# Performance work log

Measured on AMD Instinct MI355X. Metric: run time of the kernel, lower is better.

## Reference

```python
import jax, jax.numpy as jnp
import numpy as np

L, B, S, D, H, DK, F = 6, 4, 2048, 512, 8, 64, 2048


def setup_inputs() -> dict:
    key = jax.random.key(0)
    ks = iter(jax.random.split(key, 40))
    def rn(shape, scale=0.02):
        return jax.random.normal(next(ks), shape, jnp.float32) * scale
    inp = {
        "x": jax.random.normal(next(ks), (B, S, D), jnp.float32),
        "enc": jax.random.normal(next(ks), (B, S, D), jnp.float32),
    }
    for pre in ("sa", "ca"):
        inp[f"{pre}_wq"] = rn((L, D, H * DK)); inp[f"{pre}_bq"] = jnp.zeros((L, H * DK), jnp.float32)
        inp[f"{pre}_wk"] = rn((L, D, H * DK)); inp[f"{pre}_bk"] = jnp.zeros((L, H * DK), jnp.float32)
        inp[f"{pre}_wv"] = rn((L, D, H * DK)); inp[f"{pre}_bv"] = jnp.zeros((L, H * DK), jnp.float32)
        inp[f"{pre}_wo"] = rn((L, H * DK, D)); inp[f"{pre}_bo"] = jnp.zeros((L, D), jnp.float32)
    for i in (1, 2, 3):
        inp[f"ln{i}_g"] = jnp.ones((L, D), jnp.float32)
        inp[f"ln{i}_b"] = jnp.zeros((L, D), jnp.float32)
    inp["ff_w1"] = rn((L, D, F)); inp["ff_b1"] = jnp.zeros((L, F), jnp.float32)
    inp["ff_w2"] = rn((L, F, D)); inp["ff_b2"] = jnp.zeros((L, D), jnp.float32)
    return inp


def _layer_norm(z, g, b, eps=1e-5):
    m = z.mean(-1, keepdims=True)
    v = z.var(-1, keepdims=True)
    return (z - m) * jax.lax.rsqrt(v + eps) * g + b


def _mha(q_in, kv_in, wq, bq, wk, bk, wv, bv, wo, bo, causal_bias):
    b, s, _ = q_in.shape
    Q = (q_in @ wq + bq).reshape(b, s, H, DK)   # [B,S,H,DK]
    K = (kv_in @ wk + bk).reshape(b, s, H, DK)
    V = (kv_in @ wv + bv).reshape(b, s, H, DK)
    scores = jnp.einsum("bqhd,bkhd->bhqk", Q, K) / jnp.float32(DK) ** 0.5
    if causal_bias is not None:
        scores = scores + causal_bias  # additive -inf above diagonal
    w = jax.nn.softmax(scores, axis=-1)
    att = jnp.einsum("bhqk,bkhd->bqhd", w, V).reshape(b, s, H * DK)
    return att @ wo + bo


def reference(x, enc, sa_wq, sa_bq, sa_wk, sa_bk, sa_wv, sa_bv, sa_wo, sa_bo,
              ca_wq, ca_bq, ca_wk, ca_bk, ca_wv, ca_bv, ca_wo, ca_bo,
              ln1_g, ln1_b, ln2_g, ln2_b, ln3_g, ln3_b,
              ff_w1, ff_b1, ff_w2, ff_b2):
    s = x.shape[1]
    causal_bias = jnp.triu(jnp.full((s, s), -jnp.inf, jnp.float32), 1)

    params = (sa_wq, sa_bq, sa_wk, sa_bk, sa_wv, sa_bv, sa_wo, sa_bo,
              ca_wq, ca_bq, ca_wk, ca_bk, ca_wv, ca_bv, ca_wo, ca_bo,
              ln1_g, ln1_b, ln2_g, ln2_b, ln3_g, ln3_b,
              ff_w1, ff_b1, ff_w2, ff_b2)

    def block(h, p):
        (swq, sbq, swk, sbk, swv, sbv, swo, sbo,
         cwq, cbq, cwk, cbk, cwv, cbv, cwo, cbo,
         g1, b1, g2, b2, g3, b3, w1, bb1, w2, bb2) = p
        # masked self-attention + residual + LN  (faithful to source)
        x1 = _layer_norm(h + _mha(h, h, swq, sbq, swk, sbk, swv, sbv, swo, sbo, causal_bias), g1, b1)
        # cross-attention; residual comes from the BLOCK INPUT h (source bug kept)
        y = _layer_norm(h + _mha(x1, enc, cwq, cbq, cwk, cbk, cwv, cbv, cwo, cbo, None), g2, b2)
        # FFN; residual from x1 (source bug kept)
        out = _layer_norm(x1 + (jax.nn.relu(y @ w1 + bb1) @ w2 + bb2), g3, b3)
        return out, None

    out, _ = jax.lax.scan(block, x, params)
    return out
```

## Files before the change

kernel.cpp:

```cpp
#include <hip/hip_runtime.h>
#include <stdint.h>

#define LCOUNT 6
#define BB 4
#define SS 2048
#define DD 512
#define HH 8
#define DKK 64
#define FFDIM 2048
#define MM (BB*SS)

typedef __attribute__((ext_vector_type(8))) __bf16 bf16x8;
typedef __attribute__((ext_vector_type(4))) float f32x4;
typedef unsigned short u16;

__device__ __forceinline__ u16 f2bf(float f) {
  union { __bf16 h; u16 u; } v; v.h = (__bf16)f; return v.u;
}
__device__ __forceinline__ float bf2f(u16 u) {
  union { uint32_t u; float f; } v; v.u = ((uint32_t)u) << 16;
  return v.f;
}

__device__ __forceinline__ void gload_lds16(const u16* gsrc, u16* ldst) {
  __builtin_amdgcn_global_load_lds((const __attribute__((address_space(1))) char*)gsrc,
                                   (__attribute__((address_space(3))) char*)ldst, 16, 0, 0);
}

__global__ __launch_bounds__(256) void f2bf_kernel(const float* __restrict__ in,
                                                   u16* __restrict__ outp, int n) {
  int i = (blockIdx.x * 256 + threadIdx.x) * 8;
  if (i >= n) return;
  float4 a = *(const float4*)&in[i];
  float4 b = *(const float4*)&in[i + 4];
  union { u16 us[8]; uint4 v; } pk;
  pk.us[0] = f2bf(a.x); pk.us[1] = f2bf(a.y); pk.us[2] = f2bf(a.z); pk.us[3] = f2bf(a.w);
  pk.us[4] = f2bf(b.x); pk.us[5] = f2bf(b.y); pk.us[6] = f2bf(b.z); pk.us[7] = f2bf(b.w);
  *(uint4*)&outp[i] = pk.v;
}

__global__ __launch_bounds__(256) void bias_cat(const float* a, const float* b, const float* c,
                                                float* dst, int n, int total) {
  int i = blockIdx.x * 256 + threadIdx.x;
  if (i >= total) return;
  int parts = (c != nullptr) ? 3 : 2;
  int per = parts * n;
  int l = i / per, cc = i % per;
  const float* s = cc < n ? a : (cc < 2 * n ? b : c);
  dst[i] = s[l * n + (cc % n)];
}

__global__ __launch_bounds__(256) void wtrans(const float* __restrict__ W,
                                              u16* __restrict__ Wt, int K_, int N_,
                                              size_t lstride) {
  __shared__ float tile[64 * 65];
  const int l = blockIdx.z;
  const float* Wl = W + (size_t)l * K_ * N_;
  u16* Wtl = Wt + (size_t)l * lstride;
  const int n0 = blockIdx.x * 64, k0 = blockIdx.y * 64;
  const int tid = threadIdx.x;
  const int r = tid >> 2, c4 = (tid & 3) * 16;
#pragma unroll
  for (int j = 0; j < 16; j += 4) {
    float4 v = *(const float4*)&Wl[(size_t)(k0 + r) * N_ + n0 + c4 + j];
    tile[r * 65 + c4 + j + 0] = v.x;
    tile[r * 65 + c4 + j + 1] = v.y;
    tile[r * 65 + c4 + j + 2] = v.z;
    tile[r * 65 + c4 + j + 3] = v.w;
  }
  __syncthreads();
  const int nr = tid >> 2, kc = (tid & 3) * 16;
#pragma unroll
  for (int half = 0; half < 2; ++half) {
    union { u16 us[8]; uint4 v; } pk;
#pragma unroll
    for (int e = 0; e < 8; ++e) pk.us[e] = f2bf(tile[(kc + half * 8 + e) * 65 + nr]);
    *(uint4*)&Wtl[(size_t)(n0 + nr) * K_ + k0 + kc + half * 8] = pk.v;
  }
}

struct WtBatch {
  const float* src[8];
  u16* dst[8];
  unsigned long long lstr[8];
};
__global__ __launch_bounds__(256) void wtrans8(WtBatch wb) {
  __shared__ float tile[64 * 65];
  const int z = blockIdx.z;
  const int slot = z / 6, l = z - slot * 6;
  const float* Wl = wb.src[slot] + (size_t)l * 512 * 512;
  u16* Wtl = wb.dst[slot] + (size_t)l * wb.lstr[slot];
  const int n0 = blockIdx.x * 64, k0 = blockIdx.y * 64;
  const int tid = threadIdx.x;
  const int r = tid >> 2, c4 = (tid & 3) * 16;
#pragma unroll
  for (int j = 0; j < 16; j += 4) {
    float4 v = *(const float4*)&Wl[(size_t)(k0 + r) * 512 + n0 + c4 + j];
    tile[r * 65 + c4 + j + 0] = v.x;
    tile[r * 65 + c4 + j + 1] = v.y;
    tile[r * 65 + c4 + j + 2] = v.z;
    tile[r * 65 + c4 + j + 3] = v.w;
  }
  __syncthreads();
  const int nr = tid >> 2, kc = (tid & 3) * 16;
#pragma unroll
  for (int half = 0; half < 2; ++half) {
    union { u16 us[8]; uint4 v; } pk;
#pragma unroll
    for (int e = 0; e < 8; ++e) pk.us[e] = f2bf(tile[(kc + half * 8 + e) * 65 + nr]);
    *(uint4*)&Wtl[(size_t)(n0 + nr) * 512 + k0 + kc + half * 8] = pk.v;
  }
}

template <int BMT, int BNT, int BKT, bool RELU, bool VT>
__global__ __launch_bounds__(256)
void gemm_bt(const u16* __restrict__ A, const u16* __restrict__ Bt,
             const float* __restrict__ bias, u16* __restrict__ C,
             int N_, int K_, int CS, u16* __restrict__ vt, int vtc0,
             const u16* __restrict__ A2, int a2col) {
  constexpr int MR = BMT / 32;
  constexpr int NR = BNT / 32;
  constexpr int CH = BKT / 8;
  constexpr int RPR = 2048 / BKT;
  constexpr int KS = BKT / 32;
  __shared__ u16 As[BMT * BKT];
  __shared__ u16 Bs[BNT * BKT];
  const int tid = threadIdx.x;
  const int wid = tid >> 6, lane = tid & 63;
  const int l15 = lane & 15, g = lane >> 4;
  const int wr = wid >> 1, wc = wid & 1;
  const int lrow = (CH == 8) ? (lane >> 3) : (lane >> 4);
  const int lch  = lane & (CH - 1);
  const int wrows = 64 / CH;
  const int lin = blockIdx.x + gridDim.x * blockIdx.y;
  const int nwg = gridDim.x * gridDim.y;
  const int swz = (lin & 7) * (nwg >> 3) + (lin >> 3);
  const int brow = (swz / gridDim.x) * BMT;
  const int bcol = (swz % gridDim.x) * BNT;
  const u16* Ap = (A2 != nullptr && bcol >= a2col) ? A2 : A;

  f32x4 acc[MR][NR];
#pragma unroll
  for (int m = 0; m < MR; ++m)
#pragma unroll
    for (int n = 0; n < NR; ++n) acc[m][n] = (f32x4){0.f, 0.f, 0.f, 0.f};

  for (int kt = 0; kt < K_; kt += BKT) {
#pragma unroll
    for (int r = 0; r < BMT / RPR; ++r) {
      int row = r * RPR + wid * wrows + lrow;
      int slot = lch ^ (row & 7);
      gload_lds16(Ap + (size_t)(brow + row) * K_ + kt + slot * 8,
                  &As[r * 2048 + wid * 512]);
    }
#pragma unroll
    for (int r = 0; r < BNT / RPR; ++r) {
      int row = r * RPR + wid * wrows + lrow;
      int slot = lch ^ (row & 7);
      gload_lds16(Bt + (size_t)(bcol + row) * K_ + kt + slot * 8,
                  &Bs[r * 2048 + wid * 512]);
    }
    __syncthreads();
#pragma unroll
    for (int ks = 0; ks < KS; ++ks) {
      bf16x8 af[MR], bfr[NR];
#pragma unroll
      for (int m = 0; m < MR; ++m) {
        int row = wr * (BMT / 2) + m * 16 + l15;
        int slot = (ks * 4 + g) ^ (row & 7);
        af[m] = *(const bf16x8*)&As[row * BKT + slot * 8];
      }
#pragma unroll
      for (int n = 0; n < NR; ++n) {
        int row = wc * (BNT / 2) + n * 16 + l15;
        int slot = (ks * 4 + g) ^ (row & 7);
        bfr[n] = *(const bf16x8*)&Bs[row * BKT + slot * 8];
      }
#pragma unroll
      for (int m = 0; m < MR; ++m)
#pragma unroll
        for (int n = 0; n < NR; ++n)
          acc[m][n] = __builtin_amdgcn_mfma_f32_16x16x32_bf16(af[m], bfr[n], acc[m][n], 0, 0, 0);
    }
    __syncthreads();
  }
#pragma unroll
  for (int n = 0; n < NR; ++n) {
    int col = bcol + wc * (BNT / 2) + n * 16 + l15;
    float bv = bias ? bias[col] : 0.f;
    if (VT && col >= vtc0) {
      int hh = (col - vtc0) >> 6, dd = (col - vtc0) & 63;
#pragma unroll
      for (int m = 0; m < MR; ++m) {
        int s0g = brow + wr * (BMT / 2) + m * 16 + g * 4;
        int bb = s0g >> 11, ss = s0g & (SS - 1);
        union { u16 us[4]; uint2 v; } pk;
#pragma unroll
        for (int r = 0; r < 4; ++r) pk.us[r] = f2bf(acc[m][n][r] + bv);
        *(uint2*)&vt[(((size_t)(bb * HH + hh)) * DKK + dd) * SS + ss] = pk.v;
      }
    } else {
#pragma unroll
      for (int m = 0; m < MR; ++m) {
#pragma unroll
        for (int r = 0; r < 4; ++r) {
          int rowg = brow + wr * (BMT / 2) + m * 16 + g * 4 + r;
          float v = acc[m][n][r] + bv;
          if (RELU) v = fmaxf(v, 0.f);
          C[(size_t)rowg * CS + col] = f2bf(v);
        }
      }
    }
  }
}

template <bool CAUSAL>
__global__ __launch_bounds__(256, 4)
void attn_kernel(const u16* __restrict__ Qm, const u16* __restrict__ Km,
                 const u16* __restrict__ Vt, u16* __restrict__ Om, int qks) {
  __shared__ u16 Ks[2][64 * 64];
  __shared__ u16 Vs[2][64 * 64];
  __shared__ u16 Ps[4][16 * 64];
  const int lin = blockIdx.x;
  const int bh = (lin & 7) * 4 + ((lin >> 3) >> 5);
  const int qc = (lin >> 3) & 31;
  const int qb = (qc & 1) ? (31 - (qc >> 1)) : (qc >> 1);
  const int h = bh & 7, b = bh >> 3;
  const int tid = threadIdx.x, wid = tid >> 6, lane = tid & 63;
  const int l15 = lane & 15, g = lane >> 4;
  const int qstart = qb * 64;
  const size_t qbase = ((size_t)b * SS) * qks + h * DKK;
  const size_t vtbase = (size_t)(b * HH + h) * DKK * SS;
  const size_t obase = ((size_t)b * SS) * DD + h * DKK;
  u16* psw = &Ps[wid][0];
  const int srow = wid * 8 + (lane >> 3);
  const int sslot = lane & 7;
  const int qg = qstart + wid * 16 + l15;
  const int pswz = (l15 & 7) << 1;
  const float SC = 0.18033688f;

  const u16* kp = Km + qbase;
  const u16* vp = Vt + vtbase;

  bf16x8 qf[2];
#pragma unroll
  for (int ks = 0; ks < 2; ++ks)
    qf[ks] = *(const bf16x8*)&Qm[qbase + (size_t)qg * qks + ks * 32 + g * 8];

  f32x4 oacc[4];
#pragma unroll
  for (int nb = 0; nb < 4; ++nb) oacc[nb] = (f32x4){0.f, 0.f, 0.f, 0.f};
  float m_run = -3.0e38f, l_run = 0.f;

  const int T = CAUSAL ? (qb + 1) : (SS / 64);

#pragma unroll
  for (int r = 0; r < 2; ++r) {
    int row = r * 32 + srow;
    int slot = sslot ^ (row & 7);
    gload_lds16(kp + (size_t)row * qks + slot * 8, &Ks[0][r * 2048 + wid * 512]);
    gload_lds16(vp + (size_t)row * SS + slot * 8, &Vs[0][r * 2048 + wid * 512]);
  }
  __syncthreads();

  int cur = 0;
  for (int t = 0; t < T; ++t) {
    const int kstart = t * 64;
    if (t + 1 < T) {
#pragma unroll
      for (int r = 0; r < 2; ++r) {
        int row = r * 32 + srow;
        int slot = sslot ^ (row & 7);
        gload_lds16(kp + (size_t)(kstart + 64 + row) * qks + slot * 8,
                    &Ks[cur ^ 1][r * 2048 + wid * 512]);
        gload_lds16(vp + (size_t)row * SS + kstart + 64 + slot * 8,
                    &Vs[cur ^ 1][r * 2048 + wid * 512]);
      }
    }
    f32x4 sacc[4];
#pragma unroll
    for (int nb = 0; nb < 4; ++nb) sacc[nb] = (f32x4){0.f, 0.f, 0.f, 0.f};
    __builtin_amdgcn_s_setprio(1);
#pragma unroll
    for (int nb = 0; nb < 4; ++nb) {
      int row = nb * 16 + l15;
#pragma unroll
      for (int ks = 0; ks < 2; ++ks) {
        bf16x8 kf = *(const bf16x8*)&Ks[cur][row * 64 + (((ks * 4 + g) ^ (row & 7)) * 8)];
        sacc[nb] = __builtin_amdgcn_mfma_f32_16x16x32_bf16(kf, qf[ks], sacc[nb], 0, 0, 0);
      }
    }
    __builtin_amdgcn_s_setprio(0);
    if (CAUSAL && t == T - 1) {
#pragma unroll
      for (int nb = 0; nb < 4; ++nb)
#pragma unroll
        for (int r = 0; r < 4; ++r)
          if ((kstart + nb * 16 + g * 4 + r) > qg) sacc[nb][r] = -3.0e38f;
    }
    f32x4 m4 = sacc[0];
#pragma unroll
    for (int nb = 1; nb < 4; ++nb) {
      m4[0] = fmaxf(m4[0], sacc[nb][0]); m4[1] = fmaxf(m4[1], sacc[nb][1]);
      m4[2] = fmaxf(m4[2], sacc[nb][2]); m4[3] = fmaxf(m4[3], sacc[nb][3]);
    }
    float mx = fmaxf(fmaxf(m4[0], m4[1]), fmaxf(m4[2], m4[3]));
    mx = fmaxf(mx, __shfl_xor(mx, 16));
    mx = fmaxf(mx, __shfl_xor(mx, 32));
    const bool skip = __all(mx <= m_run + 64.0f);
    float mnew = skip ? m_run : fmaxf(m_run, mx);
    float mc = mnew * SC;
    float s = 0.f;
#pragma unroll
    for (int nb = 0; nb < 4; ++nb) {
#pragma unroll
      for (int r = 0; r < 4; ++r) {
        float e = __builtin_amdgcn_exp2f(sacc[nb][r] * SC - mc);
        sacc[nb][r] = e; s += e;
      }
    }
    s += __shfl_xor(s, 16);
    s += __shfl_xor(s, 32);
    if (skip) {
      l_run += s;
    } else {
      float resc = __builtin_amdgcn_exp2f((m_run - mnew) * SC);
      l_run = l_run * resc + s;
      m_run = mnew;
      float ro[4];
#pragma unroll
      for (int r = 0; r < 4; ++r) ro[r] = __shfl(resc, g * 4 + r);
#pragma unroll
      for (int nb = 0; nb < 4; ++nb)
#pragma unroll
        for (int r = 0; r < 4; ++r) oacc[nb][r] *= ro[r];
    }
#pragma unroll
    for (int nb = 0; nb < 4; ++nb) {
      union { u16 us[4]; uint2 v; } pk;
#pragma unroll
      for (int r = 0; r < 4; ++r) pk.us[r] = f2bf(sacc[nb][r]);
      int cp = (nb * 4 + g) ^ pswz;
      *(uint2*)&psw[l15 * 64 + cp * 4] = pk.v;
    }
    bf16x8 pf[2];
#pragma unroll
    for (int ks = 0; ks < 2; ++ks) {
      int cp0 = (8 * ks + 2 * g) ^ pswz;
      pf[ks] = *(const bf16x8*)&psw[l15 * 64 + cp0 * 4];
    }
    __builtin_amdgcn_s_setprio(1);
#pragma unroll
    for (int nb = 0; nb < 4; ++nb) {
      int row = nb * 16 + l15;
#pragma unroll
      for (int ks = 0; ks < 2; ++ks) {
        bf16x8 vf = *(const bf16x8*)&Vs[cur][row * 64 + (((ks * 4 + g) ^ (row & 7)) * 8)];
        oacc[nb] = __builtin_amdgcn_mfma_f32_16x16x32_bf16(pf[ks], vf, oacc[nb], 0, 0, 0);
      }
    }
    __builtin_amdgcn_s_setprio(0);
    __syncthreads();
    cur ^= 1;
  }
  float linv = 1.f / l_run;
  float io[4];
#pragma unroll
  for (int r = 0; r < 4; ++r) io[r] = __shfl(linv, g * 4 + r);
#pragma unroll
  for (int nb = 0; nb < 4; ++nb) {
#pragma unroll
    for (int r = 0; r < 4; ++r) {
      Om[obase + (size_t)(qstart + wid * 16 + g * 4 + r) * DD + nb * 16 + l15] =
          f2bf(oacc[nb][r] * io[r]);
    }
  }
}

__global__ __launch_bounds__(256)
void ln_kernel(const u16* __restrict__ A, const u16* __restrict__ Bv,
               const float* __restrict__ gamma, const float* __restrict__ beta,
               u16* __restrict__ out_bf, float* __restrict__ out_f32) {
  const int row = blockIdx.x * 4 + (threadIdx.x >> 6);
  const int lane = threadIdx.x & 63;
  uint4 av = *(const uint4*)&A[(size_t)row * DD + lane * 8];
  uint4 bv = *(const uint4*)&Bv[(size_t)row * DD + lane * 8];
  const u16* au = (const u16*)&av;
  const u16* bu = (const u16*)&bv;
  float z[8], s = 0.f, s2 = 0.f;
#pragma unroll
  for (int j = 0; j < 8; ++j) {
    float x = bf2f(au[j]) + bf2f(bu[j]);
    z[j] = x; s += x; s2 += x * x;
  }
#pragma unroll
  for (int off = 1; off < 64; off <<= 1) {
    s += __shfl_xor(s, off);
    s2 += __shfl_xor(s2, off);
  }
  float mean = s * (1.f / 512.f);
  float var = s2 * (1.f / 512.f) - mean * mean;
  float rs = rsqrtf(var + 1e-5f);
  union { u16 us[8]; uint4 v; } pk;
#pragma unroll
  for (int j = 0; j < 8; ++j) {
    float o = (z[j] - mean) * rs * gamma[lane * 8 + j] + beta[lane * 8 + j];
    pk.us[j] = f2bf(o);
    if (out_f32) out_f32[(size_t)row * DD + lane * 8 + j] = o;
  }
  *(uint4*)&out_bf[(size_t)row * DD + lane * 8] = pk.v;
}

extern "C" void kernel_launch(void* const* d_in, const int* in_sizes, int n_in,
                              void* d_out, int out_size, void* d_ws, size_t ws_size,
                              hipStream_t stream) {
  const float* x   = (const float*)d_in[0];
  const float* enc = (const float*)d_in[1];
  const float* sa_w[4] = {(const float*)d_in[2], (const float*)d_in[4], (const float*)d_in[6], (const float*)d_in[8]};
  const float* sa_b[4] = {(const float*)d_in[3], (const float*)d_in[5], (const float*)d_in[7], (const float*)d_in[9]};
  const float* ca_w[4] = {(const float*)d_in[10], (const float*)d_in[12], (const float*)d_in[14], (const float*)d_in[16]};
  const float* ca_b[4] = {(const float*)d_in[11], (const float*)d_in[13], (const float*)d_in[15], (const float*)d_in[17]};
  const float* ln_g[3] = {(const float*)d_in[18], (const float*)d_in[20], (const float*)d_in[22]};
  const float* ln_b[3] = {(const float*)d_in[19], (const float*)d_in[21], (const float*)d_in[23]};
  const float* ffw1 = (const float*)d_in[24];
  const float* ffb1 = (const float*)d_in[25];
  const float* ffw2 = (const float*)d_in[26];
  const float* ffb2 = (const float*)d_in[27];

  char* ws = (char*)d_ws;
  size_t o = 0;
  auto take = [&](size_t bytes) {
    void* p = ws + o;
    o += (bytes + 255) & ~(size_t)255;
    return p;
  };
  u16* wqkv  = (u16*)take((size_t)LCOUNT * 1536 * 512 * 2);
  u16* wca   = (u16*)take((size_t)LCOUNT * 1536 * 512 * 2);
  u16* wosa  = (u16*)take((size_t)LCOUNT * 512 * 512 * 2);
  u16* woca  = (u16*)take((size_t)LCOUNT * 512 * 512 * 2);
  u16* w1t   = (u16*)take((size_t)LCOUNT * 512 * 2048 * 2);
  u16* w2t   = (u16*)take((size_t)LCOUNT * 2048 * 512 * 2);
  float* bqkv = (float*)take((size_t)LCOUNT * 1536 * 4);
  float* bca  = (float*)take((size_t)LCOUNT * 1536 * 4);
  u16* Hb   = (u16*)take((size_t)MM * 512 * 2);
  u16* Eb   = (u16*)take((size_t)MM * 512 * 2);
  u16* QKVb = (u16*)take((size_t)MM * 1536 * 2);
  u16* Ab   = (u16*)take((size_t)MM * 512 * 2);
  u16* Pb   = (u16*)take((size_t)MM * 512 * 2);
  u16* X1b  = (u16*)take((size_t)MM * 512 * 2);
  u16* Yb   = (u16*)take((size_t)MM * 512 * 2);
  u16* Fb   = (u16*)take((size_t)MM * 2048 * 2);
  u16* Vtb  = Fb;

  f2bf_kernel<<<2048, 256, 0, stream>>>(x, Hb, MM * 512);
  f2bf_kernel<<<2048, 256, 0, stream>>>(enc, Eb, MM * 512);
  WtBatch wb;
  wb.src[0] = sa_w[0]; wb.dst[0] = wqkv;              wb.lstr[0] = (size_t)1536 * 512;
  wb.src[1] = sa_w[1]; wb.dst[1] = wqkv + 512 * 512;  wb.lstr[1] = (size_t)1536 * 512;
  wb.src[2] = sa_w[2]; wb.dst[2] = wqkv + 1024 * 512; wb.lstr[2] = (size_t)1536 * 512;
  wb.src[3] = sa_w[3]; wb.dst[3] = wosa;              wb.lstr[3] = (size_t)512 * 512;
  wb.src[4] = ca_w[0]; wb.dst[4] = wca;               wb.lstr[4] = (size_t)1536 * 512;
  wb.src[5] = ca_w[1]; wb.dst[5] = wca + 512 * 512;   wb.lstr[5] = (size_t)1536 * 512;
  wb.src[6] = ca_w[2]; wb.dst[6] = wca + 1024 * 512;  wb.lstr[6] = (size_t)1536 * 512;
  wb.src[7] = ca_w[3]; wb.dst[7] = woca;              wb.lstr[7] = (size_t)512 * 512;
  wtrans8<<<dim3(8, 8, 48), 256, 0, stream>>>(wb);
  wtrans<<<dim3(32, 8, LCOUNT), 256, 0, stream>>>(ffw1, w1t, 512, 2048, (size_t)2048 * 512);
  wtrans<<<dim3(8, 32, LCOUNT), 256, 0, stream>>>(ffw2, w2t, 2048, 512, (size_t)512 * 2048);
  bias_cat<<<36, 256, 0, stream>>>(sa_b[0], sa_b[1], sa_b[2], bqkv, 512, LCOUNT * 1536);
  bias_cat<<<36, 256, 0, stream>>>(ca_b[0], ca_b[1], ca_b[2], bca, 512, LCOUNT * 1536);

  for (int l = 0; l < LCOUNT; ++l) {
    const size_t w512 = (size_t)l * 512 * 512;
    const size_t wff = (size_t)l * 512 * 2048;
    gemm_bt<128, 128, 64, false, true><<<dim3(12, 64), 256, 0, stream>>>(
        Hb, wqkv + (size_t)l * 1536 * 512, bqkv + l * 1536, QKVb, 1536, 512, 1536, Vtb, 1024,
        nullptr, 0);
    attn_kernel<true><<<dim3(1024), 256, 0, stream>>>(QKVb, QKVb + 512, Vtb, Ab, 1536);
    gemm_bt<64, 128, 128, false, false><<<dim3(4, 128), 256, 0, stream>>>(
        Ab, wosa + w512, sa_b[3] + l * 512, Pb, 512, 512, 512, nullptr, 0, nullptr, 0);
    ln_kernel<<<MM / 4, 256, 0, stream>>>(Hb, Pb, ln_g[0] + l * 512, ln_b[0] + l * 512, X1b, nullptr);
    gemm_bt<128, 128, 64, false, true><<<dim3(12, 64), 256, 0, stream>>>(
        X1b, wca + (size_t)l * 1536 * 512, bca + l * 1536, QKVb, 1536, 512, 1536, Vtb, 1024,
        Eb, 512);
    attn_kernel<false><<<dim3(1024), 256, 0, stream>>>(QKVb, QKVb + 512, Vtb, Ab, 1536);
    gemm_bt<64, 128, 128, false, false><<<dim3(4, 128), 256, 0, stream>>>(
        Ab, woca + w512, ca_b[3] + l * 512, Pb, 512, 512, 512, nullptr, 0, nullptr, 0);
    ln_kernel<<<MM / 4, 256, 0, stream>>>(Hb, Pb, ln_g[1] + l * 512, ln_b[1] + l * 512, Yb, nullptr);
    gemm_bt<128, 128, 64, true, false><<<dim3(16, 64), 256, 0, stream>>>(
        Yb, w1t + wff, ffb1 + l * 2048, Fb, 2048, 512, 2048, nullptr, 0, nullptr, 0);
    gemm_bt<64, 128, 128, false, false><<<dim3(4, 128), 256, 0, stream>>>(
        Fb, w2t + wff, ffb2 + l * 512, Pb, 512, 2048, 512, nullptr, 0, nullptr, 0);
    ln_kernel<<<MM / 4, 256, 0, stream>>>(X1b, Pb, ln_g[2] + l * 512, ln_b[2] + l * 512, Hb,
                                          (l == LCOUNT - 1) ? (float*)d_out : nullptr);
  }
}
```

Before: 1.797 ms.

## Fuse output projection GEMMs with bias, residual add and LayerNorm

Adds a gemm_ln kernel in which each block computes 16 full rows of 512 output columns. In the epilogue it adds the bias and residual, reduces the row statistics across waves through shared memory, and writes the normalized bf16 and optional fp32 output. This replaces the three gemm_bt plus ln_kernel pairs per layer, removing the Pb intermediate round trip and three launches per layer. In exchange, the 16-row tiles stream the whole weight slab through LDS for each block, giving much less operand reuse and no double buffering. That is especially costly for the K=2048 FFN down-projection.

Result: faster. 1.750 ms (-2.7%).

```diff
diff --git a/kernel.cpp b/kernel.cpp
--- a/kernel.cpp
+++ b/kernel.cpp
@@ -214,6 +214,115 @@
   }
 }
 
+__global__ __launch_bounds__(256)
+void gemm_ln(const u16* __restrict__ A, const u16* __restrict__ Bt,
+             const float* __restrict__ bias, const u16* __restrict__ Res,
+             const float* __restrict__ gamma, const float* __restrict__ beta,
+             u16* __restrict__ Out, float* __restrict__ Ofp, int K_) {
+  __shared__ u16 As[16 * 64];
+  __shared__ u16 Bs[512 * 64];
+  __shared__ float red[4][16][2];
+  const int tid = threadIdx.x;
+  const int wid = tid >> 6, lane = tid & 63;
+  const int l15 = lane & 15, g = lane >> 4;
+  const int lin = blockIdx.x;
+  const int swz = (lin & 7) * (gridDim.x >> 3) + (lin >> 3);
+  const int brow = swz * 16;
+  const int lrow8 = lane >> 3, lch = lane & 7;
+
+  f32x4 acc[8];
+#pragma unroll
+  for (int n = 0; n < 8; ++n) acc[n] = (f32x4){0.f, 0.f, 0.f, 0.f};
+
+  for (int kt = 0; kt < K_; kt += 64) {
+#pragma unroll
+    for (int r = 0; r < 17; ++r) {
+      int u = wid + 4 * r;
+      if (u < 66) {
+        if (u < 2) {
+          int row = u * 8 + lrow8;
+          int slot = lch ^ (row & 7);
+          gload_lds16(A + (size_t)(brow + row) * K_ + kt + slot * 8, &As[u * 512]);
+        } else {
+          int row = (u - 2) * 8 + lrow8;
+          int slot = lch ^ (row & 7);
+          gload_lds16(Bt + (size_t)row * K_ + kt + slot * 8, &Bs[(u - 2) * 512]);
+        }
+      }
+    }
+    __syncthreads();
+#pragma unroll
+    for (int ks = 0; ks < 2; ++ks) {
+      bf16x8 af = *(const bf16x8*)&As[l15 * 64 + (((ks * 4 + g) ^ (l15 & 7)) * 8)];
+#pragma unroll
+      for (int n = 0; n < 8; ++n) {
+        int c = wid * 128 + n * 16 + l15;
+        bf16x8 bfr = *(const bf16x8*)&Bs[c * 64 + (((ks * 4 + g) ^ (c & 7)) * 8)];
+        acc[n] = __builtin_amdgcn_mfma_f32_16x16x32_bf16(af, bfr, acc[n], 0, 0, 0);
+      }
+    }
+    __syncthreads();
+  }
+#pragma unroll
+  for (int rd = 0; rd < 4; ++rd) {
+    int off = rd * 2048 + tid * 8;
+    int row = off >> 9, col = off & 511;
+    uint4 v = *(const uint4*)&Res[(size_t)(brow + row) * DD + col];
+    *(uint4*)&Bs[row * 520 + col] = v;
+  }
+  __syncthreads();
+  float z[8][4];
+  float s[4] = {0.f, 0.f, 0.f, 0.f}, s2[4] = {0.f, 0.f, 0.f, 0.f};
+#pragma unroll
+  for (int n = 0; n < 8; ++n) {
+    int col = wid * 128 + n * 16 + l15;
+    float bv = bias[col];
+#pragma unroll
+    for (int r = 0; r < 4; ++r) {
+      int rl = g * 4 + r;
+      float x = acc[n][r] + bv + bf2f(Bs[rl * 520 + col]);
+      z[n][r] = x; s[r] += x; s2[r] += x * x;
+    }
+  }
+#pragma unroll
+  for (int r = 0; r < 4; ++r) {
+    s[r] += __shfl_xor(s[r], 1);  s2[r] += __shfl_xor(s2[r], 1);
+    s[r] += __shfl_xor(s[r], 2);  s2[r] += __shfl_xor(s2[r], 2);
+    s[r] += __shfl_xor(s[r], 4);  s2[r] += __shfl_xor(s2[r], 4);
+    s[r] += __shfl_xor(s[r], 8);  s2[r] += __shfl_xor(s2[r], 8);
+  }
+  if (l15 == 0) {
+#pragma unroll
+    for (int r = 0; r < 4; ++r) {
+      red[wid][g * 4 + r][0] = s[r];
+      red[wid][g * 4 + r][1] = s2[r];
+    }
+  }
+  __syncthreads();
+  float mean[4], rs[4];
+#pragma unroll
+  for (int r = 0; r < 4; ++r) {
+    int rl = g * 4 + r;
+    float ts  = red[0][rl][0] + red[1][rl][0] + red[2][rl][0] + red[3][rl][0];
+    float ts2 = red[0][rl][1] + red[1][rl][1] + red[2][rl][1] + red[3][rl][1];
+    float mn = ts * (1.f / 512.f);
+    float var = ts2 * (1.f / 512.f) - mn * mn;
+    mean[r] = mn; rs[r] = rsqrtf(var + 1e-5f);
+  }
+#pragma unroll
+  for (int n = 0; n < 8; ++n) {
+    int col = wid * 128 + n * 16 + l15;
+    float gm = gamma[col], bt = beta[col];
+#pragma unroll
+    for (int r = 0; r < 4; ++r) {
+      int rowg = brow + g * 4 + r;
+      float o = (z[n][r] - mean[r]) * rs[r] * gm + bt;
+      Out[(size_t)rowg * DD + col] = f2bf(o);
+      if (Ofp) Ofp[(size_t)rowg * DD + col] = o;
+    }
+  }
+}
+
 template <bool CAUSAL>
 __global__ __launch_bounds__(256, 4)
 void attn_kernel(const u16* __restrict__ Qm, const u16* __restrict__ Km,
@@ -377,40 +486,6 @@
   }
 }
 
-__global__ __launch_bounds__(256)
-void ln_kernel(const u16* __restrict__ A, const u16* __restrict__ Bv,
-               const float* __restrict__ gamma, const float* __restrict__ beta,
-               u16* __restrict__ out_bf, float* __restrict__ out_f32) {
-  const int row = blockIdx.x * 4 + (threadIdx.x >> 6);
-  const int lane = threadIdx.x & 63;
-  uint4 av = *(const uint4*)&A[(size_t)row * DD + lane * 8];
-  uint4 bv = *(const uint4*)&Bv[(size_t)row * DD + lane * 8];
-  const u16* au = (const u16*)&av;
-  const u16* bu = (const u16*)&bv;
-  float z[8], s = 0.f, s2 = 0.f;
-#pragma unroll
-  for (int j = 0; j < 8; ++j) {
-    float x = bf2f(au[j]) + bf2f(bu[j]);
-    z[j] = x; s += x; s2 += x * x;
-  }
-#pragma unroll
-  for (int off = 1; off < 64; off <<= 1) {
-    s += __shfl_xor(s, off);
-    s2 += __shfl_xor(s2, off);
-  }
-  float mean = s * (1.f / 512.f);
-  float var = s2 * (1.f / 512.f) - mean * mean;
-  float rs = rsqrtf(var + 1e-5f);
-  union { u16 us[8]; uint4 v; } pk;
-#pragma unroll
-  for (int j = 0; j < 8; ++j) {
-    float o = (z[j] - mean) * rs * gamma[lane * 8 + j] + beta[lane * 8 + j];
-    pk.us[j] = f2bf(o);
-    if (out_f32) out_f32[(size_t)row * DD + lane * 8 + j] = o;
-  }
-  *(uint4*)&out_bf[(size_t)row * DD + lane * 8] = pk.v;
-}
-
 extern "C" void kernel_launch(void* const* d_in, const int* in_sizes, int n_in,
                               void* d_out, int out_size, void* d_ws, size_t ws_size,
                               hipStream_t stream) {
@@ -446,7 +521,6 @@
   u16* Eb   = (u16*)take((size_t)MM * 512 * 2);
   u16* QKVb = (u16*)take((size_t)MM * 1536 * 2);
   u16* Ab   = (u16*)take((size_t)MM * 512 * 2);
-  u16* Pb   = (u16*)take((size_t)MM * 512 * 2);
   u16* X1b  = (u16*)take((size_t)MM * 512 * 2);
   u16* Yb   = (u16*)take((size_t)MM * 512 * 2);
   u16* Fb   = (u16*)take((size_t)MM * 2048 * 2);
@@ -476,21 +550,21 @@
         Hb, wqkv + (size_t)l * 1536 * 512, bqkv + l * 1536, QKVb, 1536, 512, 1536, Vtb, 1024,
         nullptr, 0);
     attn_kernel<true><<<dim3(1024), 256, 0, stream>>>(QKVb, QKVb + 512, Vtb, Ab, 1536);
-    gemm_bt<64, 128, 128, false, false><<<dim3(4, 128), 256, 0, stream>>>(
-        Ab, wosa + w512, sa_b[3] + l * 512, Pb, 512, 512, 512, nullptr, 0, nullptr, 0);
-    ln_kernel<<<MM / 4, 256, 0, stream>>>(Hb, Pb, ln_g[0] + l * 512, ln_b[0] + l * 512, X1b, nullptr);
+    gemm_ln<<<dim3(512), 256, 0, stream>>>(Ab, wosa + w512, sa_b[3] + l * 512, Hb,
+                                           ln_g[0] + l * 512, ln_b[0] + l * 512,
+                                           X1b, nullptr, 512);
     gemm_bt<128, 128, 64, false, true><<<dim3(12, 64), 256, 0, stream>>>(
         X1b, wca + (size_t)l * 1536 * 512, bca + l * 1536, QKVb, 1536, 512, 1536, Vtb, 1024,
         Eb, 512);
     attn_kernel<false><<<dim3(1024), 256, 0, stream>>>(QKVb, QKVb + 512, Vtb, Ab, 1536);
-    gemm_bt<64, 128, 128, false, false><<<dim3(4, 128), 256, 0, stream>>>(
-        Ab, woca + w512, ca_b[3] + l * 512, Pb, 512, 512, 512, nullptr, 0, nullptr, 0);
-    ln_kernel<<<MM / 4, 256, 0, stream>>>(Hb, Pb, ln_g[1] + l * 512, ln_b[1] + l * 512, Yb, nullptr);
+    gemm_ln<<<dim3(512), 256, 0, stream>>>(Ab, woca + w512, ca_b[3] + l * 512, Hb,
+                                           ln_g[1] + l * 512, ln_b[1] + l * 512,
+                                           Yb, nullptr, 512);
     gemm_bt<128, 128, 64, true, false><<<dim3(16, 64), 256, 0, stream>>>(
         Yb, w1t + wff, ffb1 + l * 2048, Fb, 2048, 512, 2048, nullptr, 0, nullptr, 0);
-    gemm_bt<64, 128, 128, false, false><<<dim3(4, 128), 256, 0, stream>>>(
-        Fb, w2t + wff, ffb2 + l * 512, Pb, 512, 2048, 512, nullptr, 0, nullptr, 0);
-    ln_kernel<<<MM / 4, 256, 0, stream>>>(X1b, Pb, ln_g[2] + l * 512, ln_b[2] + l * 512, Hb,
-                                          (l == LCOUNT - 1) ? (float*)d_out : nullptr);
-  }
-}
+    gemm_ln<<<dim3(512), 256, 0, stream>>>(Fb, w2t + wff, ffb2 + l * 512, X1b,
+                                           ln_g[2] + l * 512, ln_b[2] + l * 512,
+                                           Hb, (l == LCOUNT - 1) ? (float*)d_out : nullptr,
+                                           2048);
+  }
+}
```
